# Kernel optimization log

Hardware: AMD Instinct MI355X
Metric: run time of the kernel (lower is better)

## Reference

```python
import jax, jax.numpy as jnp
import numpy as np

EMBED = 2048
N_HEAD = 32
N_KV = 8
HEAD_DIM = 64
GROUP = N_HEAD // N_KV


def _rope_tables(seq_len, head_dim):
    inv_freq = 1.0 / (10000.0 ** (jnp.arange(0, head_dim, 2, dtype=jnp.float32) / head_dim))
    ang = jnp.arange(seq_len, dtype=jnp.float32)[:, None] * inv_freq[None, :]  # [S, D/2]
    ang = jnp.concatenate([ang, ang], axis=-1)  # [S, D]
    return jnp.cos(ang), jnp.sin(ang)


def apply_rope(x, cos, sin, offset=0):
    # x: [B, H, S, D]
    S, D = x.shape[2], x.shape[3]
    x1, x2 = x[..., : D // 2], x[..., D // 2 :]
    c = cos[offset : offset + S][None, None]
    s = sin[offset : offset + S][None, None]
    rotated = jnp.concatenate([-x2, x1], axis=-1)
    return (x * c + rotated * s).astype(x.dtype)


def setup_inputs() -> dict:
    key = jax.random.key(0)
    kx, kq, kk, kv, ko = jax.random.split(key, 5)
    B, S = 2, 2048
    x = jax.random.normal(kx, (B, S, EMBED), dtype=jnp.float32)
    mask = jnp.triu(jnp.ones((S, S), dtype=bool), k=1)  # causal: True = masked
    cos, sin = _rope_tables(S, HEAD_DIM)
    std = 0.02
    Wq = jax.random.normal(kq, (EMBED, EMBED), dtype=jnp.float32) * std
    Wk = jax.random.normal(kk, (EMBED, N_KV * HEAD_DIM), dtype=jnp.float32) * std
    Wv = jax.random.normal(kv, (EMBED, N_KV * HEAD_DIM), dtype=jnp.float32) * std
    Wo = jax.random.normal(ko, (EMBED, EMBED), dtype=jnp.float32) * std
    return {"x": x, "mask": mask, "cos": cos, "sin": sin,
            "Wq": Wq, "Wk": Wk, "Wv": Wv, "Wo": Wo}


def reference(x, mask, cos, sin, Wq, Wk, Wv, Wo):
    B, S, E = x.shape
    # projections (no bias)
    q = (x @ Wq).reshape(B, S, N_HEAD, HEAD_DIM).transpose(0, 2, 1, 3)  # [B,H,S,D]
    k = (x @ Wk).reshape(B, S, N_KV, HEAD_DIM).transpose(0, 2, 1, 3)    # [B,G,S,D]
    v = (x @ Wv).reshape(B, S, N_KV, HEAD_DIM).transpose(0, 2, 1, 3)    # [B,G,S,D]
    q = apply_rope(q, cos, sin, offset=0)
    k = apply_rope(k, cos, sin, offset=0)
    next_k, next_v = k, v  # kv cache to return
    # GQA: head h uses kv group h // GROUP; avoid repeat_interleave via reshape
    qg = q.reshape(B, N_KV, GROUP, S, HEAD_DIM)
    scores = jnp.einsum('bgjsd,bgtd->bgjst', qg, k) / np.float32(np.sqrt(HEAD_DIM))
    scores = jnp.where(mask[None, None, None], -jnp.inf, scores)
    attn = jax.nn.softmax(scores, axis=-1)
    out = jnp.einsum('bgjst,bgtd->bgjsd', attn, v)          # [B,G,group,S,D]
    out = out.reshape(B, N_HEAD, S, HEAD_DIM).transpose(0, 2, 1, 3).reshape(B, S, E)
    return out @ Wo, next_k, next_v
```

## Files before the change

kernel.cpp:

```cpp
#include <hip/hip_runtime.h>
#include <hip/hip_bf16.h>
#include <math.h>

#define NH 32
#define NKV 8
#define HD 64
#define B_ 2
#define S_ 2048
#define E_ 2048
#define M_ 4096

typedef unsigned short ushort_t;
typedef __attribute__((ext_vector_type(8))) short short8;
typedef __attribute__((ext_vector_type(4))) short short4v;
typedef __attribute__((ext_vector_type(4))) float floatx4;

__device__ inline unsigned short f2bf(float f) {
  unsigned int u = __float_as_uint(f);
  return (unsigned short)((u + 0x7FFFu + ((u >> 16) & 1u)) >> 16);
}

__device__ inline float fexp2(float x) {
  float r;
  asm("v_exp_f32 %0, %1" : "=v"(r) : "v"(x));
  return r;
}

__device__ inline void ld_lds16(const void* g, void* l) {
  __builtin_amdgcn_global_load_lds((__attribute__((address_space(1))) void*)g,
                                   (__attribute__((address_space(3))) void*)l, 16, 0, 0);
}

__global__ __launch_bounds__(256) void cast_x(const float* __restrict__ x,
                                              ushort_t* __restrict__ xb) {
  size_t i = ((size_t)blockIdx.x * 256 + threadIdx.x) * 8;
  float4 a = *(const float4*)(x + i);
  float4 b = *(const float4*)(x + i + 4);
  short8 o;
  o[0] = (short)f2bf(a.x); o[1] = (short)f2bf(a.y);
  o[2] = (short)f2bf(a.z); o[3] = (short)f2bf(a.w);
  o[4] = (short)f2bf(b.x); o[5] = (short)f2bf(b.y);
  o[6] = (short)f2bf(b.z); o[7] = (short)f2bf(b.w);
  *(short8*)(xb + i) = o;
}

__global__ __launch_bounds__(256) void transpose_w(const float* __restrict__ in,
                                                   ushort_t* __restrict__ out,
                                                   int R, int C) {
  __shared__ float tile[32][33];
  int c0 = blockIdx.x * 32, r0 = blockIdx.y * 32;
  int x = threadIdx.x, y0 = threadIdx.y;
  for (int i = 0; i < 4; i++) {
    int r = y0 + i * 8;
    tile[r][x] = in[(size_t)(r0 + r) * C + c0 + x];
  }
  __syncthreads();
  for (int i = 0; i < 4; i++) {
    int r = y0 + i * 8;
    out[(size_t)(c0 + r) * R + r0 + x] = f2bf(tile[x][r]);
  }
}

__global__ __launch_bounds__(256) void transpose_v(const float* __restrict__ outv,
                                                   ushort_t* __restrict__ vt) {
  __shared__ float t64[64][65];
  int bg = blockIdx.y;
  int tt = blockIdx.x;
  int s0 = tt * 64;
  int tid = threadIdx.x;
  size_t ibase = (size_t)bg * S_ * HD + (size_t)s0 * HD;
  for (int i = tid; i < 1024; i += 256) {
    int sr = i >> 4, dc = (i & 15) * 4;
    float4 v = *(const float4*)(outv + ibase + (size_t)sr * HD + dc);
    t64[sr][dc] = v.x; t64[sr][dc + 1] = v.y; t64[sr][dc + 2] = v.z; t64[sr][dc + 3] = v.w;
  }
  __syncthreads();
  size_t obase = ((size_t)bg * 32 + tt) * 4096;
  for (int i = tid; i < 512; i += 256) {
    int d = i >> 3, ss = (i & 7) * 8;
    short8 o;
#pragma unroll
    for (int e = 0; e < 8; e++) o[e] = (short)f2bf(t64[ss + e][d]);
    *(short8*)(vt + obase + d * 64 + (ss ^ ((d & 7) << 3))) = o;
  }
}

__device__ __forceinline__ void gemm128_core(const ushort_t* __restrict__ Ag,
                                             const ushort_t* __restrict__ Bg,
                                             floatx4 (&acc)[4][4]) {
  __shared__ __align__(16) ushort_t As[2][128][64];
  __shared__ __align__(16) ushort_t Bs[2][128][64];
  int tid = threadIdx.x;
  int w = tid >> 6, lane = tid & 63;
  int wm = (w >> 1) * 64, wn = (w & 1) * 64;
  int lr = lane & 15, quad = lane >> 4;
  int sx = lr & 7;
  char* Asb = (char*)As;
  char* Bsb = (char*)Bs;

  size_t so[4];
#pragma unroll
  for (int s = 0; s < 4; s++)
    so[s] = (size_t)(w * 32 + s * 8 + (lane >> 3)) * 4096 + (size_t)(((lane & 7) ^ (lane >> 3)) * 16);
  const char* abase = (const char*)Ag;
  const char* bbase = (const char*)Bg;

#define STAGE128(buf, kt)                                          \
  do {                                                             \
    size_t ko = (size_t)(kt) * 128;                                \
    char* Ad = Asb + (buf) * 16384 + w * 4096;                     \
    char* Bd = Bsb + (buf) * 16384 + w * 4096;                     \
    _Pragma("unroll") for (int s = 0; s < 4; s++) {                \
      ld_lds16(abase + so[s] + ko, Ad + s * 1024);                 \
      ld_lds16(bbase + so[s] + ko, Bd + s * 1024);                 \
    }                                                              \
  } while (0)

  STAGE128(0, 0);
  __syncthreads();

  int cur = 0;
  for (int kt = 0; kt < 32; kt++) {
    if (kt < 31) STAGE128(cur ^ 1, kt + 1);
    const char* Ab = Asb + cur * 16384;
    const char* Bb = Bsb + cur * 16384;
    short8 af[4][2], bfr[4][2];
#pragma unroll
    for (int i = 0; i < 4; i++) {
      size_t rb = (size_t)(wm + i * 16 + lr) * 128;
#pragma unroll
      for (int ks = 0; ks < 2; ks++)
        af[i][ks] = *(const short8*)(Ab + rb + (((ks * 4 + quad) ^ sx) << 4));
    }
#pragma unroll
    for (int j = 0; j < 4; j++) {
      size_t rb = (size_t)(wn + j * 16 + lr) * 128;
#pragma unroll
      for (int ks = 0; ks < 2; ks++)
        bfr[j][ks] = *(const short8*)(Bb + rb + (((ks * 4 + quad) ^ sx) << 4));
    }
#pragma unroll
    for (int i = 0; i < 4; i++)
#pragma unroll
      for (int j = 0; j < 4; j++) {
        acc[i][j] = __builtin_amdgcn_mfma_f32_16x16x32_bf16(af[i][0], bfr[j][0], acc[i][j], 0, 0, 0);
        acc[i][j] = __builtin_amdgcn_mfma_f32_16x16x32_bf16(af[i][1], bfr[j][1], acc[i][j], 0, 0, 0);
      }
    __syncthreads();
    cur ^= 1;
  }
#undef STAGE128
}

__global__ __launch_bounds__(256) void gemm_qkv(const ushort_t* __restrict__ xb,
                                                const ushort_t* __restrict__ WT,
                                                ushort_t* __restrict__ qbf,
                                                float* __restrict__ outk,
                                                ushort_t* __restrict__ kbf,
                                                float* __restrict__ outv,
                                                const float* __restrict__ cosP,
                                                const float* __restrict__ sinP) {
  int o = blockIdx.y * 24 + blockIdx.x;
  int swz = (o & 7) * 96 + (o >> 3);
  int n0 = (swz % 24) * 128, m0 = (swz / 24) * 128;
  int tid = threadIdx.x;
  int w = tid >> 6, lane = tid & 63;
  int wm = (w >> 1) * 64, wn = (w & 1) * 64;
  int lr = lane & 15, quad = lane >> 4;

  floatx4 acc[4][4] = {};
  gemm128_core(xb + (size_t)m0 * 2048, WT + (size_t)n0 * 2048, acc);

  if (n0 < 2048) {
    const float QS = 0.125f * 1.4426950408889634f;
#pragma unroll
    for (int i = 0; i < 4; i++)
#pragma unroll
      for (int j = 0; j < 2; j++) {
        int d = j * 16 + lr;
#pragma unroll
        for (int r = 0; r < 4; r++) {
          int row = m0 + wm + i * 16 + quad * 4 + r;
          int s = row & (S_ - 1);
          float c = cosP[s * 64 + d], sn = sinP[s * 64 + d];
          float x1 = acc[i][j][r], x2 = acc[i][j + 2][r];
          size_t oo = (size_t)row * 2048 + n0 + wn + d;
          qbf[oo] = f2bf((x1 * c - x2 * sn) * QS);
          qbf[oo + 32] = f2bf((x2 * c + x1 * sn) * QS);
        }
      }
  } else if (n0 < 2560) {
    int h = (n0 - 2048 + wn) >> 6;
#pragma unroll
    for (int i = 0; i < 4; i++)
#pragma unroll
      for (int j = 0; j < 2; j++) {
        int d = j * 16 + lr;
#pragma unroll
        for (int r = 0; r < 4; r++) {
          int row = m0 + wm + i * 16 + quad * 4 + r;
          int s = row & (S_ - 1), b = row >> 11;
          float c = cosP[s * 64 + d], sn = sinP[s * 64 + d];
          float x1 = acc[i][j][r], x2 = acc[i][j + 2][r];
          float y1 = x1 * c - x2 * sn, y2 = x2 * c + x1 * sn;
          size_t rowb = ((size_t)(b * NKV + h) * S_ + s) * 64;
          int xr = (s & 7) << 3;
          outk[rowb + d] = y1; outk[rowb + d + 32] = y2;
          kbf[rowb + (d ^ xr)] = f2bf(y1);
          kbf[rowb + ((d + 32) ^ xr)] = f2bf(y2);
        }
      }
  } else {
    int h = (n0 - 2560 + wn) >> 6;
#pragma unroll
    for (int i = 0; i < 4; i++)
#pragma unroll
      for (int j = 0; j < 4; j++) {
        int d = j * 16 + lr;
#pragma unroll
        for (int r = 0; r < 4; r++) {
          int row = m0 + wm + i * 16 + quad * 4 + r;
          int s = row & (S_ - 1), b = row >> 11;
          outv[((size_t)(b * NKV + h) * S_ + s) * 64 + d] = acc[i][j][r];
        }
      }
  }
}

__global__ __launch_bounds__(256) void gemm_o(const ushort_t* __restrict__ ctx,
                                              const ushort_t* __restrict__ WoT,
                                              float* __restrict__ y) {
  int o = blockIdx.y * 16 + blockIdx.x;
  int swz = (o & 7) * 64 + (o >> 3);
  int n0 = (swz % 16) * 128, m0 = (swz / 16) * 128;
  int tid = threadIdx.x;
  int w = tid >> 6, lane = tid & 63;
  int wm = (w >> 1) * 64, wn = (w & 1) * 64;
  int lr = lane & 15, quad = lane >> 4;

  floatx4 acc[4][4] = {};
  gemm128_core(ctx + (size_t)m0 * 2048, WoT + (size_t)n0 * 2048, acc);

#pragma unroll
  for (int i = 0; i < 4; i++)
#pragma unroll
    for (int j = 0; j < 4; j++) {
      int row = m0 + wm + i * 16 + quad * 4;
      int col = n0 + wn + j * 16 + lr;
#pragma unroll
      for (int r = 0; r < 4; r++)
        y[(size_t)(row + r) * 2048 + col] = acc[i][j][r];
    }
}

__global__ __launch_bounds__(256, 4) void attn2(ushort_t* __restrict__ q,
                                                const ushort_t* __restrict__ k,
                                                const ushort_t* __restrict__ vt) {
  __shared__ __align__(16) ushort_t KV[2][2][64][64];
  __shared__ __align__(16) ushort_t Ps[4][16][64];
  int bh = blockIdx.x;
  int qt = 31 - blockIdx.y;
  int b = bh >> 5, h = bh & 31, g = h >> 2;
  int tid = threadIdx.x;
  int w = tid >> 6, lane = tid & 63;
  int lr = lane & 15, quad = lane >> 4;

  int qg = qt * 64 + w * 16 + lr;
  short8 aq0, aq1;
  {
    const ushort_t* qp = q + ((size_t)(b * S_ + qg) * NH + h) * HD;
    aq0 = *(const short8*)(qp + quad * 8);
    aq1 = *(const short8*)(qp + 32 + quad * 8);
  }
  floatx4 od[4] = {};
  float mi = -INFINITY, li = 0.f;

  const char* ksrc = (const char*)(k + (size_t)(b * NKV + g) * S_ * HD) + w * 2048 + lane * 16;
  const char* vsrc = (const char*)(vt + (size_t)(b * NKV + g) * S_ * HD) + w * 2048 + lane * 16;
  char* dB = (char*)&KV[0][0][0][0] + w * 2048;

  int sw = (lr & 7) << 4;
  int ro0 = (quad * 16) ^ sw;
  int ro1 = (64 + quad * 16) ^ sw;
  char* Pw = (char*)&Ps[0][0][0] + w * 2048;

  ld_lds16(ksrc, dB);
  ld_lds16(ksrc + 1024, dB + 1024);
  ld_lds16(vsrc, dB + 8192);
  ld_lds16(vsrc + 1024, dB + 8192 + 1024);
  asm volatile("s_waitcnt vmcnt(0)" ::: "memory");
  __syncthreads();

  int cur = 0;
  for (int t = 0; t <= qt; t++) {
    if (t < qt) {
      const char* kn = ksrc + (size_t)(t + 1) * 8192;
      const char* vn = vsrc + (size_t)(t + 1) * 8192;
      char* d = dB + (cur ^ 1) * 16384;
      ld_lds16(kn, d); ld_lds16(kn + 1024, d + 1024);
      ld_lds16(vn, d + 8192); ld_lds16(vn + 1024, d + 8192 + 1024);
    }
    const char* Kb = (const char*)&KV[cur][0][0][0];
    const char* Vb = (const char*)&KV[cur][1][0][0];
    floatx4 sc[4];
#pragma unroll
    for (int kn = 0; kn < 4; kn++) {
      short8 a0 = *(const short8*)(Kb + (kn * 16 + lr) * 128 + ro0);
      short8 a1 = *(const short8*)(Kb + (kn * 16 + lr) * 128 + ro1);
      floatx4 c = {};
      c = __builtin_amdgcn_mfma_f32_16x16x32_bf16(a0, aq0, c, 0, 0, 0);
      c = __builtin_amdgcn_mfma_f32_16x16x32_bf16(a1, aq1, c, 0, 0, 0);
      sc[kn] = c;
    }
    float pv[16];
#pragma unroll
    for (int kn = 0; kn < 4; kn++)
#pragma unroll
      for (int r = 0; r < 4; r++) pv[kn * 4 + r] = sc[kn][r];
    if (t == qt) {
#pragma unroll
      for (int e = 0; e < 16; e++) {
        int kg = t * 64 + (e >> 2) * 16 + quad * 4 + (e & 3);
        if (kg > qg) pv[e] = -INFINITY;
      }
    }
    float mx = pv[0];
#pragma unroll
    for (int e = 1; e < 16; e++) mx = fmaxf(mx, pv[e]);
    mx = fmaxf(mx, __shfl_xor(mx, 16));
    mx = fmaxf(mx, __shfl_xor(mx, 32));
    if (__any(mx > mi + 11.5f)) {
      float mn = fmaxf(mi, mx);
      float al = fexp2(mi - mn);
      li *= al;
#pragma unroll
      for (int dn = 0; dn < 4; dn++) {
        od[dn][0] *= al; od[dn][1] *= al; od[dn][2] *= al; od[dn][3] *= al;
      }
      mi = mn;
    }
    float ps = 0.f;
#pragma unroll
    for (int e = 0; e < 16; e++) {
      pv[e] = fexp2(pv[e] - mi);
      ps += pv[e];
    }
    ps += __shfl_xor(ps, 16);
    ps += __shfl_xor(ps, 32);
    li += ps;
#pragma unroll
    for (int kn = 0; kn < 4; kn++) {
      unsigned int u0, u1;
      asm("v_cvt_pk_bf16_f32 %0, %1, %2" : "=v"(u0) : "v"(pv[kn * 4 + 0]), "v"(pv[kn * 4 + 1]));
      asm("v_cvt_pk_bf16_f32 %0, %1, %2" : "=v"(u1) : "v"(pv[kn * 4 + 2]), "v"(pv[kn * 4 + 3]));
      uint2 uu; uu.x = u0; uu.y = u1;
      *(uint2*)(Pw + lr * 128 + ((kn * 32 + quad * 8) ^ sw)) = uu;
    }
    short8 pb0 = *(const short8*)(Pw + lr * 128 + ro0);
    short8 pb1 = *(const short8*)(Pw + lr * 128 + ro1);
#pragma unroll
    for (int dn = 0; dn < 4; dn++) {
      short8 va = *(const short8*)(Vb + (dn * 16 + lr) * 128 + ro0);
      short8 vb = *(const short8*)(Vb + (dn * 16 + lr) * 128 + ro1);
      od[dn] = __builtin_amdgcn_mfma_f32_16x16x32_bf16(va, pb0, od[dn], 0, 0, 0);
      od[dn] = __builtin_amdgcn_mfma_f32_16x16x32_bf16(vb, pb1, od[dn], 0, 0, 0);
    }
    asm volatile("s_waitcnt vmcnt(0)" ::: "memory");
    __syncthreads();
    cur ^= 1;
  }
  float inv = 1.f / li;
  ushort_t* outp = q + ((size_t)(b * S_ + qg) * NH + h) * HD;
#pragma unroll
  for (int dn = 0; dn < 4; dn++) {
    short4v u;
    u[0] = (short)f2bf(od[dn][0] * inv); u[1] = (short)f2bf(od[dn][1] * inv);
    u[2] = (short)f2bf(od[dn][2] * inv); u[3] = (short)f2bf(od[dn][3] * inv);
    *(short4v*)(outp + dn * 16 + quad * 4) = u;
  }
}

extern "C" void kernel_launch(void* const* d_in, const int* in_sizes, int n_in,
                              void* d_out, int out_size, void* d_ws, size_t ws_size,
                              hipStream_t stream) {
  const float* x = (const float*)d_in[0];
  const float* cosT = (const float*)d_in[2];
  const float* sinT = (const float*)d_in[3];
  const float* Wq = (const float*)d_in[4];
  const float* Wk = (const float*)d_in[5];
  const float* Wv = (const float*)d_in[6];
  const float* Wo = (const float*)d_in[7];

  char* ws = (char*)d_ws;
  ushort_t* WT = (ushort_t*)(ws);
  ushort_t* WoT = (ushort_t*)(ws + 12582912);
  ushort_t* xb = (ushort_t*)(ws + 20971520);
  ushort_t* qbf = (ushort_t*)(ws + 37748736);
  ushort_t* kbf = (ushort_t*)(ws + 54525952);
  ushort_t* vt = (ushort_t*)(ws + 58720256);

  float* y = (float*)d_out;
  float* outk = y + (size_t)M_ * E_;
  float* outv = outk + (size_t)B_ * NKV * S_ * HD;

  cast_x<<<dim3(4096), 256, 0, stream>>>(x, xb);
  transpose_w<<<dim3(64, 64), dim3(32, 8), 0, stream>>>(Wq, WT, 2048, 2048);
  transpose_w<<<dim3(16, 64), dim3(32, 8), 0, stream>>>(Wk, WT + 2048 * 2048, 2048, 512);
  transpose_w<<<dim3(16, 64), dim3(32, 8), 0, stream>>>(Wv, WT + 2560 * 2048, 2048, 512);
  transpose_w<<<dim3(64, 64), dim3(32, 8), 0, stream>>>(Wo, WoT, 2048, 2048);

  gemm_qkv<<<dim3(24, 32), 256, 0, stream>>>(xb, WT, qbf, outk, kbf, outv, cosT, sinT);
  transpose_v<<<dim3(32, 16), 256, 0, stream>>>(outv, vt);

  attn2<<<dim3(64, 32), 256, 0, stream>>>(qbf, kbf, vt);

  gemm_o<<<dim3(16, 32), 256, 0, stream>>>(qbf, WoT, y);
}
```

Baseline: 344.0 us.

## Use 8-wave GEMM blocks with a 4-stage LDS pipeline and explicit vmcnt waits

Both GEMM kernels now launch 512 threads per 128x128 tile, and each wave computes a 32x64 sub-tile instead of 64x64. The shared-memory staging goes from double to quad buffering, keeping three loads in flight. Explicit s_waitcnt vmcnt counts and raw s_barrier replace the per-iteration __syncthreads. The aim is more latency hiding and more waves resident per CU, at the cost of 128KB of LDS per block, which may cap occupancy at one block per CU, and fragile hand-tuned wait counts.

```diff
diff --git a/kernel.cpp b/kernel.cpp
--- a/kernel.cpp
+++ b/kernel.cpp
@@ -87,72 +87,88 @@
 
 __device__ __forceinline__ void gemm128_core(const ushort_t* __restrict__ Ag,
                                              const ushort_t* __restrict__ Bg,
-                                             floatx4 (&acc)[4][4]) {
-  __shared__ __align__(16) ushort_t As[2][128][64];
-  __shared__ __align__(16) ushort_t Bs[2][128][64];
+                                             floatx4 (&acc)[2][4]) {
+  __shared__ __align__(16) ushort_t As[4][128][64];
+  __shared__ __align__(16) ushort_t Bs[4][128][64];
   int tid = threadIdx.x;
   int w = tid >> 6, lane = tid & 63;
-  int wm = (w >> 1) * 64, wn = (w & 1) * 64;
+  int wm = (w >> 1) * 32;
+  int wn = (w & 1) * 64;
   int lr = lane & 15, quad = lane >> 4;
   int sx = lr & 7;
   char* Asb = (char*)As;
   char* Bsb = (char*)Bs;
 
-  size_t so[4];
-#pragma unroll
-  for (int s = 0; s < 4; s++)
-    so[s] = (size_t)(w * 32 + s * 8 + (lane >> 3)) * 4096 + (size_t)(((lane & 7) ^ (lane >> 3)) * 16);
+  size_t so0, so1;
+  {
+    int r0 = w * 8 + (lane >> 3);
+    int r1 = 64 + w * 8 + (lane >> 3);
+    int cs = ((lane & 7) ^ (lane >> 3)) * 16;
+    so0 = (size_t)r0 * 4096 + cs;
+    so1 = (size_t)r1 * 4096 + cs;
+  }
   const char* abase = (const char*)Ag;
   const char* bbase = (const char*)Bg;
 
-#define STAGE128(buf, kt)                                          \
-  do {                                                             \
-    size_t ko = (size_t)(kt) * 128;                                \
-    char* Ad = Asb + (buf) * 16384 + w * 4096;                     \
-    char* Bd = Bsb + (buf) * 16384 + w * 4096;                     \
-    _Pragma("unroll") for (int s = 0; s < 4; s++) {                \
-      ld_lds16(abase + so[s] + ko, Ad + s * 1024);                 \
-      ld_lds16(bbase + so[s] + ko, Bd + s * 1024);                 \
-    }                                                              \
+#define STAGE(b, kt)                                 \
+  do {                                               \
+    size_t ko = (size_t)(kt) * 128;                  \
+    char* Ad = Asb + (b) * 16384 + w * 1024;         \
+    char* Bd = Bsb + (b) * 16384 + w * 1024;         \
+    ld_lds16(abase + so0 + ko, Ad);                  \
+    ld_lds16(abase + so1 + ko, Ad + 8192);           \
+    ld_lds16(bbase + so0 + ko, Bd);                  \
+    ld_lds16(bbase + so1 + ko, Bd + 8192);           \
   } while (0)
 
-  STAGE128(0, 0);
-  __syncthreads();
-
-  int cur = 0;
-  for (int kt = 0; kt < 32; kt++) {
-    if (kt < 31) STAGE128(cur ^ 1, kt + 1);
-    const char* Ab = Asb + cur * 16384;
-    const char* Bb = Bsb + cur * 16384;
-    short8 af[4][2], bfr[4][2];
-#pragma unroll
-    for (int i = 0; i < 4; i++) {
-      size_t rb = (size_t)(wm + i * 16 + lr) * 128;
-#pragma unroll
-      for (int ks = 0; ks < 2; ks++)
-        af[i][ks] = *(const short8*)(Ab + rb + (((ks * 4 + quad) ^ sx) << 4));
-    }
-#pragma unroll
-    for (int j = 0; j < 4; j++) {
-      size_t rb = (size_t)(wn + j * 16 + lr) * 128;
-#pragma unroll
-      for (int ks = 0; ks < 2; ks++)
-        bfr[j][ks] = *(const short8*)(Bb + rb + (((ks * 4 + quad) ^ sx) << 4));
-    }
-#pragma unroll
-    for (int i = 0; i < 4; i++)
-#pragma unroll
-      for (int j = 0; j < 4; j++) {
-        acc[i][j] = __builtin_amdgcn_mfma_f32_16x16x32_bf16(af[i][0], bfr[j][0], acc[i][j], 0, 0, 0);
-        acc[i][j] = __builtin_amdgcn_mfma_f32_16x16x32_bf16(af[i][1], bfr[j][1], acc[i][j], 0, 0, 0);
-      }
-    __syncthreads();
-    cur ^= 1;
-  }
-#undef STAGE128
-}
-
-__global__ __launch_bounds__(256) void gemm_qkv(const ushort_t* __restrict__ xb,
+#define COMPUTE(kt)                                                               \
+  do {                                                                            \
+    const char* Ab = Asb + ((kt) & 3) * 16384;                                    \
+    const char* Bb = Bsb + ((kt) & 3) * 16384;                                    \
+    short8 af[2][2], bfr[4][2];                                                   \
+    _Pragma("unroll") for (int i = 0; i < 2; i++) {                               \
+      size_t rb = (size_t)(wm + i * 16 + lr) * 128;                               \
+      _Pragma("unroll") for (int ks = 0; ks < 2; ks++)                            \
+        af[i][ks] = *(const short8*)(Ab + rb + (((ks * 4 + quad) ^ sx) << 4));    \
+    }                                                                             \
+    _Pragma("unroll") for (int j = 0; j < 4; j++) {                               \
+      size_t rb = (size_t)(wn + j * 16 + lr) * 128;                               \
+      _Pragma("unroll") for (int ks = 0; ks < 2; ks++)                            \
+        bfr[j][ks] = *(const short8*)(Bb + rb + (((ks * 4 + quad) ^ sx) << 4));   \
+    }                                                                             \
+    _Pragma("unroll") for (int i = 0; i < 2; i++)                                 \
+      _Pragma("unroll") for (int j = 0; j < 4; j++) {                             \
+        acc[i][j] = __builtin_amdgcn_mfma_f32_16x16x32_bf16(af[i][0], bfr[j][0],  \
+                                                            acc[i][j], 0, 0, 0); \
+        acc[i][j] = __builtin_amdgcn_mfma_f32_16x16x32_bf16(af[i][1], bfr[j][1],  \
+                                                            acc[i][j], 0, 0, 0); \
+      }                                                                           \
+  } while (0)
+
+  STAGE(0, 0);
+  STAGE(1, 1);
+  STAGE(2, 2);
+
+  for (int kt = 0; kt < 30; kt++) {
+    asm volatile("s_waitcnt vmcnt(8)" ::: "memory");
+    __builtin_amdgcn_s_barrier();
+    __builtin_amdgcn_sched_barrier(0);
+    if (kt < 29) STAGE((kt + 3) & 3, kt + 3);
+    COMPUTE(kt);
+  }
+  asm volatile("s_waitcnt vmcnt(4)" ::: "memory");
+  __builtin_amdgcn_s_barrier();
+  __builtin_amdgcn_sched_barrier(0);
+  COMPUTE(30);
+  asm volatile("s_waitcnt vmcnt(0)" ::: "memory");
+  __builtin_amdgcn_s_barrier();
+  __builtin_amdgcn_sched_barrier(0);
+  COMPUTE(31);
+#undef STAGE
+#undef COMPUTE
+}
+
+__global__ __launch_bounds__(512) void gemm_qkv(const ushort_t* __restrict__ xb,
                                                 const ushort_t* __restrict__ WT,
                                                 ushort_t* __restrict__ qbf,
                                                 float* __restrict__ outk,
@@ -165,16 +181,16 @@
   int n0 = (swz % 24) * 128, m0 = (swz / 24) * 128;
   int tid = threadIdx.x;
   int w = tid >> 6, lane = tid & 63;
-  int wm = (w >> 1) * 64, wn = (w & 1) * 64;
+  int wm = (w >> 1) * 32, wn = (w & 1) * 64;
   int lr = lane & 15, quad = lane >> 4;
 
-  floatx4 acc[4][4] = {};
+  floatx4 acc[2][4] = {};
   gemm128_core(xb + (size_t)m0 * 2048, WT + (size_t)n0 * 2048, acc);
 
   if (n0 < 2048) {
     const float QS = 0.125f * 1.4426950408889634f;
 #pragma unroll
-    for (int i = 0; i < 4; i++)
+    for (int i = 0; i < 2; i++)
 #pragma unroll
       for (int j = 0; j < 2; j++) {
         int d = j * 16 + lr;
@@ -192,7 +208,7 @@
   } else if (n0 < 2560) {
     int h = (n0 - 2048 + wn) >> 6;
 #pragma unroll
-    for (int i = 0; i < 4; i++)
+    for (int i = 0; i < 2; i++)
 #pragma unroll
       for (int j = 0; j < 2; j++) {
         int d = j * 16 + lr;
@@ -213,7 +229,7 @@
   } else {
     int h = (n0 - 2560 + wn) >> 6;
 #pragma unroll
-    for (int i = 0; i < 4; i++)
+    for (int i = 0; i < 2; i++)
 #pragma unroll
       for (int j = 0; j < 4; j++) {
         int d = j * 16 + lr;
@@ -227,7 +243,7 @@
   }
 }
 
-__global__ __launch_bounds__(256) void gemm_o(const ushort_t* __restrict__ ctx,
+__global__ __launch_bounds__(512) void gemm_o(const ushort_t* __restrict__ ctx,
                                               const ushort_t* __restrict__ WoT,
                                               float* __restrict__ y) {
   int o = blockIdx.y * 16 + blockIdx.x;
@@ -235,14 +251,14 @@
   int n0 = (swz % 16) * 128, m0 = (swz / 16) * 128;
   int tid = threadIdx.x;
   int w = tid >> 6, lane = tid & 63;
-  int wm = (w >> 1) * 64, wn = (w & 1) * 64;
+  int wm = (w >> 1) * 32, wn = (w & 1) * 64;
   int lr = lane & 15, quad = lane >> 4;
 
-  floatx4 acc[4][4] = {};
+  floatx4 acc[2][4] = {};
   gemm128_core(ctx + (size_t)m0 * 2048, WoT + (size_t)n0 * 2048, acc);
 
 #pragma unroll
-  for (int i = 0; i < 4; i++)
+  for (int i = 0; i < 2; i++)
 #pragma unroll
     for (int j = 0; j < 4; j++) {
       int row = m0 + wm + i * 16 + quad * 4;
@@ -409,10 +425,10 @@
   transpose_w<<<dim3(16, 64), dim3(32, 8), 0, stream>>>(Wv, WT + 2560 * 2048, 2048, 512);
   transpose_w<<<dim3(64, 64), dim3(32, 8), 0, stream>>>(Wo, WoT, 2048, 2048);
 
-  gemm_qkv<<<dim3(24, 32), 256, 0, stream>>>(xb, WT, qbf, outk, kbf, outv, cosT, sinT);
+  gemm_qkv<<<dim3(24, 32), 512, 0, stream>>>(xb, WT, qbf, outk, kbf, outv, cosT, sinT);
   transpose_v<<<dim3(32, 16), 256, 0, stream>>>(outv, vt);
 
   attn2<<<dim3(64, 32), 256, 0, stream>>>(qbf, kbf, vt);
 
-  gemm_o<<<dim3(16, 32), 256, 0, stream>>>(qbf, WoT, y);
-}
+  gemm_o<<<dim3(16, 32), 512, 0, stream>>>(qbf, WoT, y);
+}
```

Result: slower. 364.5 us (+6.0%).

## Process 128-key tiles per attention iteration with MFMA priority hints

Applied to the files above, without the earlier changes.

The attention kernel now stages two 64-key K/V sub-tiles per loop iteration, so each iteration covers 128 keys. This halves the number of barrier and waitcnt sync points and the online-softmax rescale and reduce steps per key. It also wraps the MFMA sections in s_setprio to favour matrix issue. In exchange it doubles LDS use to 64KB plus a larger P buffer, drops the occupancy hint from launch bounds, and masks some extra keys on the diagonal tile.

```diff
diff --git a/kernel.cpp b/kernel.cpp
--- a/kernel.cpp
+++ b/kernel.cpp
@@ -253,11 +253,11 @@
     }
 }
 
-__global__ __launch_bounds__(256, 4) void attn2(ushort_t* __restrict__ q,
-                                                const ushort_t* __restrict__ k,
-                                                const ushort_t* __restrict__ vt) {
-  __shared__ __align__(16) ushort_t KV[2][2][64][64];
-  __shared__ __align__(16) ushort_t Ps[4][16][64];
+__global__ __launch_bounds__(256) void attn2(ushort_t* __restrict__ q,
+                                             const ushort_t* __restrict__ k,
+                                             const ushort_t* __restrict__ vt) {
+  __shared__ __align__(16) ushort_t KV[2][2][2][64][64];
+  __shared__ __align__(16) ushort_t Ps[4][16][128];
   int bh = blockIdx.x;
   int qt = 31 - blockIdx.y;
   int b = bh >> 5, h = bh & 31, g = h >> 2;
@@ -275,58 +275,66 @@
   floatx4 od[4] = {};
   float mi = -INFINITY, li = 0.f;
 
-  const char* ksrc = (const char*)(k + (size_t)(b * NKV + g) * S_ * HD) + w * 2048 + lane * 16;
-  const char* vsrc = (const char*)(vt + (size_t)(b * NKV + g) * S_ * HD) + w * 2048 + lane * 16;
-  char* dB = (char*)&KV[0][0][0][0] + w * 2048;
+  const char* kbase = (const char*)(k + (size_t)(b * NKV + g) * S_ * HD);
+  const char* vbase = (const char*)(vt + (size_t)(b * NKV + g) * S_ * HD);
+  char* KVb = (char*)&KV[0][0][0][0][0];
+  int soff = w * 2048 + lane * 16;
 
   int sw = (lr & 7) << 4;
   int ro0 = (quad * 16) ^ sw;
   int ro1 = (64 + quad * 16) ^ sw;
-  char* Pw = (char*)&Ps[0][0][0] + w * 2048;
-
-  ld_lds16(ksrc, dB);
-  ld_lds16(ksrc + 1024, dB + 1024);
-  ld_lds16(vsrc, dB + 8192);
-  ld_lds16(vsrc + 1024, dB + 8192 + 1024);
+  char* Pw = (char*)&Ps[0][0][0] + w * 4096;
+
+#define ASTAGE(buf, t)                                                                     \
+  do {                                                                                     \
+    _Pragma("unroll") for (int sub = 0; sub < 2; sub++) {                                  \
+      const char* sk = kbase + (size_t)(t) * 16384 + sub * 8192 + soff;                    \
+      const char* sv = vbase + ((size_t)(t) * 2 + sub) * 8192 + soff;                      \
+      char* dk = KVb + (buf) * 32768 + sub * 16384 + w * 2048;                             \
+      char* dv = dk + 8192;                                                                \
+      ld_lds16(sk, dk); ld_lds16(sk + 1024, dk + 1024);                                    \
+      ld_lds16(sv, dv); ld_lds16(sv + 1024, dv + 1024);                                    \
+    }                                                                                      \
+  } while (0)
+
+  int nt = (qt + 2) >> 1;
+  ASTAGE(0, 0);
   asm volatile("s_waitcnt vmcnt(0)" ::: "memory");
   __syncthreads();
 
   int cur = 0;
-  for (int t = 0; t <= qt; t++) {
-    if (t < qt) {
-      const char* kn = ksrc + (size_t)(t + 1) * 8192;
-      const char* vn = vsrc + (size_t)(t + 1) * 8192;
-      char* d = dB + (cur ^ 1) * 16384;
-      ld_lds16(kn, d); ld_lds16(kn + 1024, d + 1024);
-      ld_lds16(vn, d + 8192); ld_lds16(vn + 1024, d + 8192 + 1024);
-    }
-    const char* Kb = (const char*)&KV[cur][0][0][0];
-    const char* Vb = (const char*)&KV[cur][1][0][0];
-    floatx4 sc[4];
-#pragma unroll
-    for (int kn = 0; kn < 4; kn++) {
-      short8 a0 = *(const short8*)(Kb + (kn * 16 + lr) * 128 + ro0);
-      short8 a1 = *(const short8*)(Kb + (kn * 16 + lr) * 128 + ro1);
-      floatx4 c = {};
-      c = __builtin_amdgcn_mfma_f32_16x16x32_bf16(a0, aq0, c, 0, 0, 0);
-      c = __builtin_amdgcn_mfma_f32_16x16x32_bf16(a1, aq1, c, 0, 0, 0);
-      sc[kn] = c;
-    }
-    float pv[16];
-#pragma unroll
-    for (int kn = 0; kn < 4; kn++)
-#pragma unroll
-      for (int r = 0; r < 4; r++) pv[kn * 4 + r] = sc[kn][r];
-    if (t == qt) {
-#pragma unroll
-      for (int e = 0; e < 16; e++) {
-        int kg = t * 64 + (e >> 2) * 16 + quad * 4 + (e & 3);
+  for (int t = 0; t < nt; t++) {
+    if (t + 1 < nt) ASTAGE(cur ^ 1, t + 1);
+    const char* Tb = KVb + cur * 32768;
+    floatx4 sc[8];
+    __builtin_amdgcn_s_setprio(1);
+#pragma unroll
+    for (int sub = 0; sub < 2; sub++) {
+      const char* Kb = Tb + sub * 16384;
+#pragma unroll
+      for (int kn = 0; kn < 4; kn++) {
+        short8 a0 = *(const short8*)(Kb + (kn * 16 + lr) * 128 + ro0);
+        short8 a1 = *(const short8*)(Kb + (kn * 16 + lr) * 128 + ro1);
+        floatx4 c = {};
+        c = __builtin_amdgcn_mfma_f32_16x16x32_bf16(a0, aq0, c, 0, 0, 0);
+        c = __builtin_amdgcn_mfma_f32_16x16x32_bf16(a1, aq1, c, 0, 0, 0);
+        sc[sub * 4 + kn] = c;
+      }
+    }
+    __builtin_amdgcn_s_setprio(0);
+    float pv[32];
+#pragma unroll
+    for (int e = 0; e < 32; e++) pv[e] = sc[e >> 2][e & 3];
+    if (t == nt - 1) {
+#pragma unroll
+      for (int e = 0; e < 32; e++) {
+        int kg = t * 128 + (e >> 4) * 64 + ((e >> 2) & 3) * 16 + quad * 4 + (e & 3);
         if (kg > qg) pv[e] = -INFINITY;
       }
     }
     float mx = pv[0];
 #pragma unroll
-    for (int e = 1; e < 16; e++) mx = fmaxf(mx, pv[e]);
+    for (int e = 1; e < 32; e++) mx = fmaxf(mx, pv[e]);
     mx = fmaxf(mx, __shfl_xor(mx, 16));
     mx = fmaxf(mx, __shfl_xor(mx, 32));
     if (__any(mx > mi + 11.5f)) {
@@ -341,7 +349,7 @@
     }
     float ps = 0.f;
 #pragma unroll
-    for (int e = 0; e < 16; e++) {
+    for (int e = 0; e < 32; e++) {
       pv[e] = fexp2(pv[e] - mi);
       ps += pv[e];
     }
@@ -349,26 +357,36 @@
     ps += __shfl_xor(ps, 32);
     li += ps;
 #pragma unroll
-    for (int kn = 0; kn < 4; kn++) {
-      unsigned int u0, u1;
-      asm("v_cvt_pk_bf16_f32 %0, %1, %2" : "=v"(u0) : "v"(pv[kn * 4 + 0]), "v"(pv[kn * 4 + 1]));
-      asm("v_cvt_pk_bf16_f32 %0, %1, %2" : "=v"(u1) : "v"(pv[kn * 4 + 2]), "v"(pv[kn * 4 + 3]));
-      uint2 uu; uu.x = u0; uu.y = u1;
-      *(uint2*)(Pw + lr * 128 + ((kn * 32 + quad * 8) ^ sw)) = uu;
-    }
-    short8 pb0 = *(const short8*)(Pw + lr * 128 + ro0);
-    short8 pb1 = *(const short8*)(Pw + lr * 128 + ro1);
-#pragma unroll
-    for (int dn = 0; dn < 4; dn++) {
-      short8 va = *(const short8*)(Vb + (dn * 16 + lr) * 128 + ro0);
-      short8 vb = *(const short8*)(Vb + (dn * 16 + lr) * 128 + ro1);
-      od[dn] = __builtin_amdgcn_mfma_f32_16x16x32_bf16(va, pb0, od[dn], 0, 0, 0);
-      od[dn] = __builtin_amdgcn_mfma_f32_16x16x32_bf16(vb, pb1, od[dn], 0, 0, 0);
-    }
+    for (int sub = 0; sub < 2; sub++)
+#pragma unroll
+      for (int kn = 0; kn < 4; kn++) {
+        int e = sub * 16 + kn * 4;
+        unsigned int u0, u1;
+        asm("v_cvt_pk_bf16_f32 %0, %1, %2" : "=v"(u0) : "v"(pv[e + 0]), "v"(pv[e + 1]));
+        asm("v_cvt_pk_bf16_f32 %0, %1, %2" : "=v"(u1) : "v"(pv[e + 2]), "v"(pv[e + 3]));
+        uint2 uu; uu.x = u0; uu.y = u1;
+        *(uint2*)(Pw + lr * 256 + sub * 128 + ((kn * 32 + quad * 8) ^ sw)) = uu;
+      }
+    __builtin_amdgcn_s_setprio(1);
+#pragma unroll
+    for (int sub = 0; sub < 2; sub++) {
+      short8 pb0 = *(const short8*)(Pw + lr * 256 + sub * 128 + ro0);
+      short8 pb1 = *(const short8*)(Pw + lr * 256 + sub * 128 + ro1);
+      const char* Vb = Tb + sub * 16384 + 8192;
+#pragma unroll
+      for (int dn = 0; dn < 4; dn++) {
+        short8 va = *(const short8*)(Vb + (dn * 16 + lr) * 128 + ro0);
+        short8 vb = *(const short8*)(Vb + (dn * 16 + lr) * 128 + ro1);
+        od[dn] = __builtin_amdgcn_mfma_f32_16x16x32_bf16(va, pb0, od[dn], 0, 0, 0);
+        od[dn] = __builtin_amdgcn_mfma_f32_16x16x32_bf16(vb, pb1, od[dn], 0, 0, 0);
+      }
+    }
+    __builtin_amdgcn_s_setprio(0);
     asm volatile("s_waitcnt vmcnt(0)" ::: "memory");
     __syncthreads();
     cur ^= 1;
   }
+#undef ASTAGE
   float inv = 1.f / li;
   ushort_t* outp = q + ((size_t)(b * S_ + qg) * NH + h) * HD;
 #pragma unroll
```

After: 347.0 us. Within noise of the previous version (+0.9%).
